# Performance work log

Measured on AMD Instinct MI355X. Metric: run time of the kernel, lower is better.

Reference implementation:

```python
import jax, jax.numpy as jnp
import numpy as np

N, E, FE, H, G, L, OUT = 50000, 300000, 64, 256, 256, 4, 128
BN_EPS = 1e-5


def setup_inputs() -> dict:
    key = jax.random.key(0)
    ks = jax.random.split(key, 12)
    s = 0.05
    return dict(
        x=jax.random.normal(ks[0], (N, H), jnp.float32),
        edge_index=jax.random.randint(ks[1], (2, E), 0, N, dtype=jnp.int64),
        edge_attr=jax.random.normal(ks[2], (E, FE), jnp.float32),
        batch=jnp.sort(jax.random.randint(ks[3], (N,), 0, G, dtype=jnp.int64)),
        bond_W1=jax.random.normal(ks[4], (L, FE, H), jnp.float32) * s,
        bond_b1=jnp.zeros((L, H), jnp.float32),
        bond_W2=jax.random.normal(ks[5], (L, H, H), jnp.float32) * s,
        bond_b2=jnp.zeros((L, H), jnp.float32),
        mlp_W1=jax.random.normal(ks[6], (L, H, H), jnp.float32) * s,
        mlp_b1=jnp.zeros((L, H), jnp.float32),
        mlp_W2=jax.random.normal(ks[7], (L, H, H), jnp.float32) * s,
        mlp_b2=jnp.zeros((L, H), jnp.float32),
        eps=jnp.zeros((L,), jnp.float32),
        bn_gamma=jnp.ones((L, H), jnp.float32),
        bn_beta=jnp.zeros((L, H), jnp.float32),
        fc1_W=jax.random.normal(ks[8], (L * H, H), jnp.float32) * s,
        fc1_b=jnp.zeros((H,), jnp.float32),
        fc4_W=jax.random.normal(ks[9], (H, OUT), jnp.float32) * s,
        fc4_b=jnp.zeros((OUT,), jnp.float32),
    )


def reference(x, edge_index, edge_attr, batch,
              bond_W1, bond_b1, bond_W2, bond_b2,
              mlp_W1, mlp_b1, mlp_W2, mlp_b2,
              eps, bn_gamma, bn_beta,
              fc1_W, fc1_b, fc4_W, fc4_b):
    src, dst = edge_index[0], edge_index[1]  # x_j gathered from src, scatter-add to dst
    x_lst = []
    for l in range(L):
        # bond encoder: Linear -> ReLU -> Linear on edge features [E, FE] -> [E, H]
        e = jax.nn.relu(edge_attr @ bond_W1[l] + bond_b1[l]) @ bond_W2[l] + bond_b2[l]
        # message = relu(x_j + e), aggregate = scatter-add over destination nodes
        msg = jax.nn.relu(x[src] + e)  # [E, H]
        aggr = jax.ops.segment_sum(msg, dst, num_segments=N)  # [N, H]
        h = (1.0 + eps[l]) * x + aggr
        h = jax.nn.relu(h @ mlp_W1[l] + mlp_b1[l]) @ mlp_W2[l] + mlp_b2[l]
        h = jax.nn.relu(h)
        # BatchNorm over the node dimension (training-style batch statistics)
        mu = jnp.mean(h, axis=0)
        var = jnp.var(h, axis=0)
        x = (h - mu) * jax.lax.rsqrt(var + BN_EPS) * bn_gamma[l] + bn_beta[l]
        x_lst.append(x)
    xc = jnp.concatenate(x_lst, axis=-1)  # [N, L*H]
    # global mean pool over graphs
    sums = jax.ops.segment_sum(xc, batch, num_segments=G)  # [G, L*H]
    cnts = jax.ops.segment_sum(jnp.ones((N,), xc.dtype), batch, num_segments=G)
    pooled = sums / jnp.maximum(cnts, 1.0)[:, None]
    h = jax.nn.relu(pooled @ fc1_W + fc1_b)
    # dropout p=0.5 in eval mode -> identity
    return h @ fc4_W + fc4_b  # [G, OUT]
```

## Files before the change

### kernel.cpp

```cpp
#include <hip/hip_runtime.h>

#define NN 50000
#define NE 300000
#define FEA 64
#define HD 256
#define NG 256
#define NL 4
#define OD 128
#define SCB ((NN + 255) / 256)

typedef unsigned short u16;
typedef unsigned int u32;
typedef __attribute__((ext_vector_type(8))) short short8;
typedef __attribute__((ext_vector_type(4))) float f32x4;

__device__ __forceinline__ u16 f2h(float f) {
    union { _Float16 h; u16 u; } v; v.h = (_Float16)f; return v.u;
}
__device__ __forceinline__ float h2f(u16 u) {
    union { u16 u; _Float16 h; } v; v.u = u; return (float)v.h;
}

__global__ __launch_bounds__(256, 2) void edge_k(
    const u16* __restrict__ eattrS, const u16* __restrict__ W1t,
    const float* __restrict__ bb1, const u16* __restrict__ W2t,
    const float* __restrict__ bb2,
    const int* __restrict__ srcI, const int* __restrict__ dstI,
    const u16* __restrict__ xh, float* __restrict__ aggr)
{
    __shared__ __align__(16) u16 bufW[256 * 64];
    __shared__ __align__(16) u16 bufT[64 * 256];
    __shared__ int dstL[64];
    const int tid = threadIdx.x;
    const int lane = tid & 63;
    const int w = tid >> 6;
    const int q = lane >> 4, c15 = lane & 15;
    const int e0 = blockIdx.x * 64;

#pragma unroll
    for (int it = 0; it < 2; ++it) {
        const int i = it * 256 + tid;
        const int m = i >> 3, kb = i & 7;
        int row = e0 + m; if (row > NE - 1) row = NE - 1;
        *(short8*)&bufT[m * 64 + ((kb ^ (m & 7)) * 8)] =
            *(const short8*)(eattrS + (size_t)row * FEA + kb * 8);
    }
#pragma unroll
    for (int it = 0; it < 8; ++it) {
        const int i = it * 256 + tid;
        const int n = i >> 3, kb = i & 7;
        *(short8*)&bufW[n * 64 + ((kb ^ (n & 7)) * 8)] =
            *(const short8*)(W1t + (size_t)n * FEA + kb * 8);
    }
    if (tid < 64) {
        int er = e0 + tid;
        dstL[tid] = (er < NE) ? dstI[er] : -1;
    }
    __syncthreads();

    f32x4 acc1[4][4];
#pragma unroll
    for (int i = 0; i < 4; ++i)
#pragma unroll
        for (int j = 0; j < 4; ++j) acc1[i][j] = (f32x4)0.0f;
#pragma unroll
    for (int s = 0; s < 2; ++s) {
        short8 af[4], bf[4];
#pragma unroll
        for (int t = 0; t < 4; ++t) {
            const int kga = s * 4 + q;
            const int mm = t * 16 + c15;
            af[t] = *(const short8*)&bufT[mm * 64 + ((kga ^ (mm & 7)) * 8)];
            const int nn = w * 64 + t * 16 + c15;
            bf[t] = *(const short8*)&bufW[nn * 64 + ((kga ^ (nn & 7)) * 8)];
        }
#pragma unroll
        for (int tm = 0; tm < 4; ++tm)
#pragma unroll
            for (int tn = 0; tn < 4; ++tn)
                acc1[tm][tn] = __builtin_amdgcn_mfma_f32_16x16x32_f16(
                    af[tm], bf[tn], acc1[tm][tn], 0, 0, 0);
    }
    __syncthreads();

    {
        float b1f[4];
#pragma unroll
        for (int tn = 0; tn < 4; ++tn)
            b1f[tn] = bb1[w * 64 + tn * 16 + c15];
#pragma unroll
        for (int tm = 0; tm < 4; ++tm)
#pragma unroll
            for (int tn = 0; tn < 4; ++tn) {
                const int col = w * 64 + tn * 16 + c15;
                const int kb = col >> 3;
#pragma unroll
                for (int r = 0; r < 4; ++r) {
                    const int row = tm * 16 + q * 4 + r;
                    float v = acc1[tm][tn][r] + b1f[tn];
                    v = v > 0.0f ? v : 0.0f;
                    bufT[row * 256 + ((kb ^ (row & 7)) * 8) + (col & 7)] = f2h(v);
                }
            }
    }

    f32x4 acc2[4][4];
#pragma unroll
    for (int i = 0; i < 4; ++i)
#pragma unroll
        for (int j = 0; j < 4; ++j) acc2[i][j] = (f32x4)0.0f;
    for (int k0 = 0; k0 < 256; k0 += 64) {
#pragma unroll
        for (int it = 0; it < 8; ++it) {
            const int i = it * 256 + tid;
            const int n = i >> 3, kbl = i & 7;
            *(short8*)&bufW[n * 64 + ((kbl ^ (n & 7)) * 8)] =
                *(const short8*)(W2t + (size_t)n * HD + k0 + kbl * 8);
        }
        __syncthreads();
#pragma unroll
        for (int s = 0; s < 2; ++s) {
            short8 af[4], bf[4];
#pragma unroll
            for (int t = 0; t < 4; ++t) {
                const int mm = t * 16 + c15;
                const int kbg = (k0 >> 3) + s * 4 + q;
                af[t] = *(const short8*)&bufT[mm * 256 + ((kbg ^ (mm & 7)) * 8)];
                const int nn = w * 64 + t * 16 + c15;
                const int kga = s * 4 + q;
                bf[t] = *(const short8*)&bufW[nn * 64 + ((kga ^ (nn & 7)) * 8)];
            }
#pragma unroll
            for (int tm = 0; tm < 4; ++tm)
#pragma unroll
                for (int tn = 0; tn < 4; ++tn)
                    acc2[tm][tn] = __builtin_amdgcn_mfma_f32_16x16x32_f16(
                        af[tm], bf[tn], acc2[tm][tn], 0, 0, 0);
        }
        __syncthreads();
    }

#pragma unroll
    for (int it = 0; it < 8; ++it) {
        const int idx = it * 256 + tid;
        const int row = idx >> 5;
        const int ch = idx & 31;
        int er = e0 + row; if (er > NE - 1) er = NE - 1;
        const int sn = srcI[er];
        *(short8*)&bufW[row * 256 + ch * 8] =
            *(const short8*)(xh + (size_t)sn * HD + ch * 8);
    }
    __syncthreads();

    {
        float b2f[4];
#pragma unroll
        for (int tn = 0; tn < 4; ++tn)
            b2f[tn] = bb2[w * 64 + tn * 16 + c15];
#pragma unroll
        for (int tm = 0; tm < 4; ++tm)
#pragma unroll
            for (int r = 0; r < 4; ++r) {
                const int row = tm * 16 + q * 4 + r;
                if (e0 + row < NE) {
#pragma unroll
                    for (int tn = 0; tn < 4; ++tn) {
                        const int col = w * 64 + tn * 16 + c15;
                        float v = acc2[tm][tn][r] + b2f[tn]
                                + h2f(bufW[row * 256 + col]);
                        v = v > 0.0f ? v : 0.0f;
                        bufT[row * 256 + col] = f2h(v);
                    }
                }
            }
    }
    __syncthreads();

    {
        const int hiR = (NE - e0 < 64) ? (NE - e0) : 64;
        float s = 0.0f;
        int cur = dstL[0];
        for (int rI = 0; rI < hiR; ++rI) {
            const int d = dstL[rI];
            if (d != cur) {
                if (s != 0.0f) unsafeAtomicAdd(&aggr[(size_t)cur * HD + tid], s);
                cur = d; s = 0.0f;
            }
            s += h2f(bufT[rI * 256 + tid]);
        }
        if (cur >= 0 && s != 0.0f)
            unsafeAtomicAdd(&aggr[(size_t)cur * HD + tid], s);
    }
}

__global__ __launch_bounds__(256, 2) void node_k(
    const u16* __restrict__ xh, const float* __restrict__ aggr,
    const float* __restrict__ epsv, int l,
    const u16* __restrict__ M1t, const float* __restrict__ mb1,
    const u16* __restrict__ M2t, const float* __restrict__ mb2,
    u16* __restrict__ hb, float* __restrict__ bns, float* __restrict__ bnq)
{
    __shared__ __align__(16) u16 bufW[256 * 64];
    __shared__ __align__(16) u16 bufT[64 * 256];
    const int tid = threadIdx.x;
    const int lane = tid & 63;
    const int w = tid >> 6;
    const int q = lane >> 4, c15 = lane & 15;
    const int n0b = blockIdx.x * 64;
    const float e1 = 1.0f + epsv[l];

#pragma unroll
    for (int it = 0; it < 8; ++it) {
        const int i = it * 256 + tid;
        const int m = i >> 5, kb = i & 31;
        int row = n0b + m; if (row > NN - 1) row = NN - 1;
        const size_t base = (size_t)row * HD + kb * 8;
        short8 xv = *(const short8*)(xh + base);
        float4 a0 = *(const float4*)(aggr + base);
        float4 a1 = *(const float4*)(aggr + base + 4);
        u16 o[8];
        o[0] = f2h(e1 * h2f((u16)xv[0]) + a0.x);
        o[1] = f2h(e1 * h2f((u16)xv[1]) + a0.y);
        o[2] = f2h(e1 * h2f((u16)xv[2]) + a0.z);
        o[3] = f2h(e1 * h2f((u16)xv[3]) + a0.w);
        o[4] = f2h(e1 * h2f((u16)xv[4]) + a1.x);
        o[5] = f2h(e1 * h2f((u16)xv[5]) + a1.y);
        o[6] = f2h(e1 * h2f((u16)xv[6]) + a1.z);
        o[7] = f2h(e1 * h2f((u16)xv[7]) + a1.w);
        *(short8*)&bufT[m * 256 + ((kb ^ (m & 7)) * 8)] = *(short8*)o;
    }

    f32x4 acc1[4][4];
#pragma unroll
    for (int i = 0; i < 4; ++i)
#pragma unroll
        for (int j = 0; j < 4; ++j) acc1[i][j] = (f32x4)0.0f;
    for (int k0 = 0; k0 < 256; k0 += 64) {
#pragma unroll
        for (int it = 0; it < 8; ++it) {
            const int i = it * 256 + tid;
            const int n = i >> 3, kbl = i & 7;
            *(short8*)&bufW[n * 64 + ((kbl ^ (n & 7)) * 8)] =
                *(const short8*)(M1t + (size_t)n * HD + k0 + kbl * 8);
        }
        __syncthreads();
#pragma unroll
        for (int s = 0; s < 2; ++s) {
            short8 af[4], bf[4];
#pragma unroll
            for (int t = 0; t < 4; ++t) {
                const int mm = t * 16 + c15;
                const int kbg = (k0 >> 3) + s * 4 + q;
                af[t] = *(const short8*)&bufT[mm * 256 + ((kbg ^ (mm & 7)) * 8)];
                const int nn = w * 64 + t * 16 + c15;
                const int kga = s * 4 + q;
                bf[t] = *(const short8*)&bufW[nn * 64 + ((kga ^ (nn & 7)) * 8)];
            }
#pragma unroll
            for (int tm = 0; tm < 4; ++tm)
#pragma unroll
                for (int tn = 0; tn < 4; ++tn)
                    acc1[tm][tn] = __builtin_amdgcn_mfma_f32_16x16x32_f16(
                        af[tm], bf[tn], acc1[tm][tn], 0, 0, 0);
        }
        __syncthreads();
    }

    {
        float b1f[4];
#pragma unroll
        for (int tn = 0; tn < 4; ++tn)
            b1f[tn] = mb1[w * 64 + tn * 16 + c15];
#pragma unroll
        for (int tm = 0; tm < 4; ++tm)
#pragma unroll
            for (int tn = 0; tn < 4; ++tn) {
                const int col = w * 64 + tn * 16 + c15;
                const int kb = col >> 3;
#pragma unroll
                for (int r = 0; r < 4; ++r) {
                    const int row = tm * 16 + q * 4 + r;
                    float v = acc1[tm][tn][r] + b1f[tn];
                    v = v > 0.0f ? v : 0.0f;
                    bufT[row * 256 + ((kb ^ (row & 7)) * 8) + (col & 7)] = f2h(v);
                }
            }
    }

    f32x4 acc2[4][4];
#pragma unroll
    for (int i = 0; i < 4; ++i)
#pragma unroll
        for (int j = 0; j < 4; ++j) acc2[i][j] = (f32x4)0.0f;
    for (int k0 = 0; k0 < 256; k0 += 64) {
#pragma unroll
        for (int it = 0; it < 8; ++it) {
            const int i = it * 256 + tid;
            const int n = i >> 3, kbl = i & 7;
            *(short8*)&bufW[n * 64 + ((kbl ^ (n & 7)) * 8)] =
                *(const short8*)(M2t + (size_t)n * HD + k0 + kbl * 8);
        }
        __syncthreads();
#pragma unroll
        for (int s = 0; s < 2; ++s) {
            short8 af[4], bf[4];
#pragma unroll
            for (int t = 0; t < 4; ++t) {
                const int mm = t * 16 + c15;
                const int kbg = (k0 >> 3) + s * 4 + q;
                af[t] = *(const short8*)&bufT[mm * 256 + ((kbg ^ (mm & 7)) * 8)];
                const int nn = w * 64 + t * 16 + c15;
                const int kga = s * 4 + q;
                bf[t] = *(const short8*)&bufW[nn * 64 + ((kga ^ (nn & 7)) * 8)];
            }
#pragma unroll
            for (int tm = 0; tm < 4; ++tm)
#pragma unroll
                for (int tn = 0; tn < 4; ++tn)
                    acc2[tm][tn] = __builtin_amdgcn_mfma_f32_16x16x32_f16(
                        af[tm], bf[tn], acc2[tm][tn], 0, 0, 0);
        }
        __syncthreads();
    }

    float b2f[4];
#pragma unroll
    for (int tn = 0; tn < 4; ++tn)
        b2f[tn] = mb2[w * 64 + tn * 16 + c15];
    float ps[4] = {0, 0, 0, 0}, pq[4] = {0, 0, 0, 0};
#pragma unroll
    for (int tm = 0; tm < 4; ++tm) {
#pragma unroll
        for (int r = 0; r < 4; ++r) {
            const int grow = n0b + tm * 16 + q * 4 + r;
            if (grow < NN) {
#pragma unroll
                for (int tn = 0; tn < 4; ++tn) {
                    const int col = w * 64 + tn * 16 + c15;
                    float v = acc2[tm][tn][r] + b2f[tn];
                    v = v > 0.0f ? v : 0.0f;
                    hb[(size_t)grow * HD + col] = f2h(v);
                    ps[tn] += v; pq[tn] += v * v;
                }
            }
        }
    }
#pragma unroll
    for (int tn = 0; tn < 4; ++tn) {
        float s = ps[tn], sq = pq[tn];
        s += __shfl_down(s, 32, 64);  sq += __shfl_down(sq, 32, 64);
        s += __shfl_down(s, 16, 64);  sq += __shfl_down(sq, 16, 64);
        if (q == 0) {
            const int col = w * 64 + tn * 16 + c15;
            unsafeAtomicAdd(&bns[col], s);
            unsafeAtomicAdd(&bnq[col], sq);
        }
    }
}


__global__ void transpose_k(const float* __restrict__ in, u16* __restrict__ oh,
                            int Kw, int Nw) {
    int i = blockIdx.x * blockDim.x + threadIdx.x;
    int tot = NL * Kw * Nw;
    if (i < tot) {
        int l = i / (Kw * Nw), rem = i % (Kw * Nw);
        int k = rem / Nw, n = rem % Nw;
        oh[(size_t)l * Kw * Nw + (size_t)n * Kw + k] = f2h(in[i]);
    }
}

__global__ void cvt_k(const float* __restrict__ in, u16* __restrict__ outh, int tot) {
    int i = blockIdx.x * blockDim.x + threadIdx.x;
    if (i < tot) outh[i] = f2h(in[i]);
}

__global__ void egather_k(const float* __restrict__ eattr, const int* __restrict__ perm,
                          u16* __restrict__ eattrS) {
    int i = blockIdx.x * blockDim.x + threadIdx.x;
    if (i < NE * FEA) {
        int row = i >> 6, k = i & 63;
        eattrS[i] = f2h(eattr[(size_t)perm[row] * FEA + k]);
    }
}

__global__ void zero_layer_k(float* __restrict__ aggr, float* __restrict__ bns,
                             float* __restrict__ bnq) {
    int i = blockIdx.x * blockDim.x + threadIdx.x;
    if (i < NN * HD) aggr[i] = 0.0f;
    if (i < HD) { bns[i] = 0.0f; bnq[i] = 0.0f; }
}

__global__ void bnfin_k(const float* __restrict__ bns, const float* __restrict__ bnq,
                        const float* __restrict__ gamma, const float* __restrict__ beta,
                        int l, float* __restrict__ ab) {
    int c = threadIdx.x;
    float mu = bns[c] * (1.0f / (float)NN);
    float var = bnq[c] * (1.0f / (float)NN) - mu * mu;
    if (var < 0.0f) var = 0.0f;
    float a = gamma[l * HD + c] * rsqrtf(var + 1e-5f);
    float b = beta[l * HD + c] - mu * a;
    ab[c] = a; ab[HD + c] = b;
}

__global__ void bnapply_k(const u16* __restrict__ hb, const float* __restrict__ ab,
                          u16* __restrict__ xh) {
    int i = blockIdx.x * blockDim.x + threadIdx.x;
    if (i < NN * HD) {
        int c = i & (HD - 1);
        xh[i] = f2h(ab[c] * h2f(hb[i]) + ab[HD + c]);
    }
}


__global__ void zeroi_k(int* __restrict__ a, int n) {
    int i = blockIdx.x * blockDim.x + threadIdx.x;
    if (i < n) a[i] = 0;
}

__global__ void hist_k(const int* __restrict__ dst, int* __restrict__ hist) {
    int e = blockIdx.x * blockDim.x + threadIdx.x;
    if (e < NE) atomicAdd(&hist[dst[e]], 1);
}

__global__ void sumblk_k(const int* __restrict__ hist, int* __restrict__ psum) {
    __shared__ int red[256];
    int b = blockIdx.x, t = threadIdx.x, i = b * 256 + t;
    red[t] = (i < NN) ? hist[i] : 0;
    __syncthreads();
    for (int o = 128; o > 0; o >>= 1) {
        if (t < o) red[t] += red[t + o];
        __syncthreads();
    }
    if (t == 0) psum[b] = red[0];
}

__global__ void scanblk_k(int* __restrict__ psum) {
    __shared__ int sc[256];
    int t = threadIdx.x;
    int v = (t < SCB) ? psum[t] : 0;
    sc[t] = v; __syncthreads();
    for (int o = 1; o < 256; o <<= 1) {
        int x = (t >= o) ? sc[t - o] : 0;
        __syncthreads(); sc[t] += x; __syncthreads();
    }
    if (t < SCB) psum[t] = sc[t] - v;
}

__global__ void scanfin_k(const int* __restrict__ hist, const int* __restrict__ psum,
                          int* __restrict__ rowptr) {
    __shared__ int sc[256];
    int b = blockIdx.x, t = threadIdx.x, i = b * 256 + t;
    int v = (i < NN) ? hist[i] : 0;
    sc[t] = v; __syncthreads();
    for (int o = 1; o < 256; o <<= 1) {
        int x = (t >= o) ? sc[t - o] : 0;
        __syncthreads(); sc[t] += x; __syncthreads();
    }
    if (i < NN) rowptr[i] = psum[b] + sc[t] - v;
    if (i == NN - 1) rowptr[NN] = psum[b] + sc[t];
}

__global__ void copyi_k(const int* __restrict__ src, int* __restrict__ dst, int n) {
    int i = blockIdx.x * blockDim.x + threadIdx.x;
    if (i < n) dst[i] = src[i];
}

__global__ void scatter_k(const int* __restrict__ dst, int* __restrict__ next,
                          int* __restrict__ perm) {
    int e = blockIdx.x * blockDim.x + threadIdx.x;
    if (e < NE) {
        int p = atomicAdd(&next[dst[e]], 1);
        perm[p] = e;
    }
}

__global__ void permsd_k(const int* __restrict__ eidx, const int* __restrict__ perm,
                         int* __restrict__ srcS, int* __restrict__ dstS) {
    int i = blockIdx.x * blockDim.x + threadIdx.x;
    if (i < NE) {
        int e = perm[i];
        srcS[i] = eidx[e];
        dstS[i] = eidx[NE + e];
    }
}


__global__ void zcnt_k(int* __restrict__ cnts) {
    if (threadIdx.x < NG) cnts[threadIdx.x] = 0;
}

__global__ void count_k(const int* __restrict__ batch, int* __restrict__ cnts) {
    int i = blockIdx.x * blockDim.x + threadIdx.x;
    if (i < NN) atomicAdd(&cnts[batch[i]], 1);
}

__global__ void offs_k(const int* __restrict__ cnts, int* __restrict__ offs) {
    if (threadIdx.x == 0) {
        int a = 0;
        for (int g = 0; g < NG; ++g) { offs[g] = a; a += cnts[g]; }
        offs[NG] = a;
    }
}

__global__ void pool_layer_k(const u16* __restrict__ xh, const int* __restrict__ offs,
                             float* __restrict__ pooled, int l) {
    int g = blockIdx.x, t = threadIdx.x;
    int lo = offs[g], hi = offs[g + 1];
    float s = 0.0f;
    for (int n = lo; n < hi; ++n) s += h2f(xh[(size_t)n * HD + t]);
    int c = hi - lo; if (c < 1) c = 1;
    pooled[(size_t)g * (NL * HD) + l * HD + t] = s / (float)c;
}

__global__ void fc_k(const float* __restrict__ pooled,
                     const float* __restrict__ W1, const float* __restrict__ b1,
                     const float* __restrict__ W4, const float* __restrict__ b4,
                     float* __restrict__ out) {
    __shared__ float pl[NL * HD];
    __shared__ float hm[HD];
    int g = blockIdx.x, t = threadIdx.x;
#pragma unroll
    for (int j = 0; j < 4; ++j) pl[t + j * 256] = pooled[(size_t)g * 1024 + t + j * 256];
    __syncthreads();
    float a = b1[t];
    for (int k = 0; k < 1024; ++k) a += pl[k] * W1[k * 256 + t];
    hm[t] = a > 0.0f ? a : 0.0f;
    __syncthreads();
    if (t < OD) {
        float o = b4[t];
        for (int k = 0; k < 256; ++k) o += hm[k] * W4[k * OD + t];
        out[g * OD + t] = o;
    }
}


extern "C" void kernel_launch(void* const* d_in, const int* in_sizes, int n_in,
                              void* d_out, int out_size, void* d_ws, size_t ws_size,
                              hipStream_t stream) {
    const float* x_in  = (const float*)d_in[0];
    const int*   eidx  = (const int*)d_in[1];
    const float* eattr = (const float*)d_in[2];
    const int*   batch = (const int*)d_in[3];
    const float* bW1   = (const float*)d_in[4];
    const float* bb1   = (const float*)d_in[5];
    const float* bW2   = (const float*)d_in[6];
    const float* bb2   = (const float*)d_in[7];
    const float* mW1   = (const float*)d_in[8];
    const float* mb1   = (const float*)d_in[9];
    const float* mW2   = (const float*)d_in[10];
    const float* mb2   = (const float*)d_in[11];
    const float* epsv  = (const float*)d_in[12];
    const float* gamma = (const float*)d_in[13];
    const float* beta  = (const float*)d_in[14];
    const float* fc1W  = (const float*)d_in[15];
    const float* fc1b  = (const float*)d_in[16];
    const float* fc4W  = (const float*)d_in[17];
    const float* fc4b  = (const float*)d_in[18];
    float* out = (float*)d_out;
    (void)in_sizes; (void)n_in; (void)out_size; (void)ws_size;

    size_t off = 0;
    auto alloc = [&](size_t bytes) -> char* {
        char* r = (char*)d_ws + off;
        off = (off + bytes + 255) & ~(size_t)255;
        return r;
    };
    u16*   xh   = (u16*)alloc((size_t)NN * HD * 2);
    float* aggr = (float*)alloc((size_t)NN * HD * 4);
    u16*   hb   = (u16*)alloc((size_t)NN * HD * 2);
    u16*   eattrS = (u16*)alloc((size_t)NE * FEA * 2);
    u16*   W1t  = (u16*)alloc((size_t)NL * FEA * HD * 2);
    u16*   W2t  = (u16*)alloc((size_t)NL * HD * HD * 2);
    u16*   M1t  = (u16*)alloc((size_t)NL * HD * HD * 2);
    u16*   M2t  = (u16*)alloc((size_t)NL * HD * HD * 2);
    float* bns  = (float*)alloc(HD * 4);
    float* bnq  = (float*)alloc(HD * 4);
    float* ab   = (float*)alloc(2 * HD * 4);
    int*   cnts = (int*)alloc(NG * 4);
    int*   offs = (int*)alloc((NG + 1) * 4);
    float* pooled = (float*)alloc((size_t)NG * NL * HD * 4);
    int*   hist  = (int*)alloc((size_t)NN * 4);
    int*   psum  = (int*)alloc((size_t)SCB * 4);
    int*   rowptr = (int*)alloc((size_t)(NN + 1) * 4);
    int*   perm  = (int*)alloc((size_t)NE * 4);
    int*   srcS  = (int*)alloc((size_t)NE * 4);
    int*   dstS  = (int*)alloc((size_t)NE * 4);

    const int NEL = NN * HD;
    const int EB = (NEL + 255) / 256;
    const int NEB = (NE + 255) / 256;

    transpose_k<<<(NL * FEA * HD + 255) / 256, 256, 0, stream>>>(bW1, W1t, FEA, HD);
    transpose_k<<<(NL * HD * HD + 255) / 256, 256, 0, stream>>>(bW2, W2t, HD, HD);
    transpose_k<<<(NL * HD * HD + 255) / 256, 256, 0, stream>>>(mW1, M1t, HD, HD);
    transpose_k<<<(NL * HD * HD + 255) / 256, 256, 0, stream>>>(mW2, M2t, HD, HD);

    cvt_k<<<EB, 256, 0, stream>>>(x_in, xh, NEL);

    zeroi_k<<<(NN + 255) / 256, 256, 0, stream>>>(hist, NN);
    hist_k<<<NEB, 256, 0, stream>>>(eidx + NE, hist);
    sumblk_k<<<SCB, 256, 0, stream>>>(hist, psum);
    scanblk_k<<<1, 256, 0, stream>>>(psum);
    scanfin_k<<<SCB, 256, 0, stream>>>(hist, psum, rowptr);
    copyi_k<<<(NN + 255) / 256, 256, 0, stream>>>(rowptr, hist, NN);
    scatter_k<<<NEB, 256, 0, stream>>>(eidx + NE, hist, perm);
    permsd_k<<<NEB, 256, 0, stream>>>(eidx, perm, srcS, dstS);
    egather_k<<<(NE * FEA + 255) / 256, 256, 0, stream>>>(eattr, perm, eattrS);

    zcnt_k<<<1, 256, 0, stream>>>(cnts);
    count_k<<<(NN + 255) / 256, 256, 0, stream>>>(batch, cnts);
    offs_k<<<1, 64, 0, stream>>>(cnts, offs);

    const int EGB = (NE + 63) / 64;
    const int NGB = (NN + 63) / 64;

    for (int l = 0; l < NL; ++l) {
        zero_layer_k<<<EB, 256, 0, stream>>>(aggr, bns, bnq);
        edge_k<<<EGB, 256, 0, stream>>>(
            eattrS, W1t + (size_t)l * FEA * HD, bb1 + l * HD,
            W2t + (size_t)l * HD * HD, bb2 + l * HD,
            srcS, dstS, xh, aggr);
        node_k<<<NGB, 256, 0, stream>>>(
            xh, aggr, epsv, l,
            M1t + (size_t)l * HD * HD, mb1 + l * HD,
            M2t + (size_t)l * HD * HD, mb2 + l * HD,
            hb, bns, bnq);
        bnfin_k<<<1, HD, 0, stream>>>(bns, bnq, gamma, beta, l, ab);
        bnapply_k<<<EB, 256, 0, stream>>>(hb, ab, xh);
        pool_layer_k<<<NG, HD, 0, stream>>>(xh, offs, pooled, l);
    }
    fc_k<<<NG, 256, 0, stream>>>(pooled, fc1W, fc1b, fc4W, fc4b, out);
}
```

Measured before the change: 1.557 ms.

## Double-buffer weight staging via direct global-to-LDS loads and fuse pooling into BN apply

The edge and node GEMM kernels now stage weight tiles with global_load_lds straight into LDS, using 32-wide K chunks that are double-buffered so the next chunk loads while MFMAs run on the current one. The x[src] gather is overlapped with the last K chunk, and s_setprio is raised around the MFMA bursts. Separately, mean pooling is folded into the BN-apply kernel through per-graph atomics, with division by the count deferred to fc_k, which removes pool_layer_k and offs_k. The cost is more barriers, float atomic-order nondeterminism in pooling, and per-row batch lookups in bnapply.

```diff
diff --git a/kernel.cpp b/kernel.cpp
--- a/kernel.cpp
+++ b/kernel.cpp
@@ -19,6 +19,12 @@
 }
 __device__ __forceinline__ float h2f(u16 u) {
     union { u16 u; _Float16 h; } v; v.u = u; return (float)v.h;
+}
+
+typedef const __attribute__((address_space(1))) unsigned int gas_u32;
+typedef __attribute__((address_space(3))) unsigned int las_u32;
+__device__ __forceinline__ void gld16(const void* g, void* l) {
+    __builtin_amdgcn_global_load_lds((gas_u32*)g, (las_u32*)l, 16, 0, 0);
 }
 
 __global__ __launch_bounds__(256, 2) void edge_k(
@@ -31,30 +37,34 @@
     __shared__ __align__(16) u16 bufW[256 * 64];
     __shared__ __align__(16) u16 bufT[64 * 256];
     __shared__ int dstL[64];
+    __shared__ int srcL[64];
     const int tid = threadIdx.x;
     const int lane = tid & 63;
     const int w = tid >> 6;
     const int q = lane >> 4, c15 = lane & 15;
     const int e0 = blockIdx.x * 64;
-
+    const int wb = tid & ~63;
+
+    if (tid < 64) {
+        int er = e0 + tid;
+        int erc = er < NE ? er : NE - 1;
+        dstL[tid] = (er < NE) ? dstI[erc] : -1;
+        srcL[tid] = srcI[erc];
+    }
 #pragma unroll
     for (int it = 0; it < 2; ++it) {
         const int i = it * 256 + tid;
         const int m = i >> 3, kb = i & 7;
         int row = e0 + m; if (row > NE - 1) row = NE - 1;
-        *(short8*)&bufT[m * 64 + ((kb ^ (m & 7)) * 8)] =
-            *(const short8*)(eattrS + (size_t)row * FEA + kb * 8);
+        gld16(eattrS + (size_t)row * FEA + ((kb ^ (m & 7)) * 8),
+              &bufT[(it * 256 + wb) * 8]);
     }
 #pragma unroll
     for (int it = 0; it < 8; ++it) {
         const int i = it * 256 + tid;
         const int n = i >> 3, kb = i & 7;
-        *(short8*)&bufW[n * 64 + ((kb ^ (n & 7)) * 8)] =
-            *(const short8*)(W1t + (size_t)n * FEA + kb * 8);
-    }
-    if (tid < 64) {
-        int er = e0 + tid;
-        dstL[tid] = (er < NE) ? dstI[er] : -1;
+        gld16(W1t + (size_t)n * FEA + ((kb ^ (n & 7)) * 8),
+              &bufW[(it * 256 + wb) * 8]);
     }
     __syncthreads();
 
@@ -74,14 +84,29 @@
             const int nn = w * 64 + t * 16 + c15;
             bf[t] = *(const short8*)&bufW[nn * 64 + ((kga ^ (nn & 7)) * 8)];
         }
+        __builtin_amdgcn_s_setprio(1);
 #pragma unroll
         for (int tm = 0; tm < 4; ++tm)
 #pragma unroll
             for (int tn = 0; tn < 4; ++tn)
                 acc1[tm][tn] = __builtin_amdgcn_mfma_f32_16x16x32_f16(
                     af[tm], bf[tn], acc1[tm][tn], 0, 0, 0);
-    }
-    __syncthreads();
+        __builtin_amdgcn_s_setprio(0);
+    }
+    __syncthreads();
+
+    auto stageW2 = [&](int cc) {
+        const int k0c = cc * 32;
+        const int hB = (cc & 1) * 1024;
+#pragma unroll
+        for (int it = 0; it < 4; ++it) {
+            const int i = it * 256 + tid;
+            const int n = i >> 2, j = i & 3;
+            gld16(W2t + (size_t)n * HD + k0c + ((j ^ ((n >> 1) & 3)) * 8),
+                  &bufW[(hB + it * 256 + wb) * 8]);
+        }
+    };
+    stageW2(0);
 
     {
         float b1f[4];
@@ -103,77 +128,76 @@
                 }
             }
     }
+    __syncthreads();
 
     f32x4 acc2[4][4];
 #pragma unroll
     for (int i = 0; i < 4; ++i)
 #pragma unroll
         for (int j = 0; j < 4; ++j) acc2[i][j] = (f32x4)0.0f;
-    for (int k0 = 0; k0 < 256; k0 += 64) {
-#pragma unroll
-        for (int it = 0; it < 8; ++it) {
-            const int i = it * 256 + tid;
-            const int n = i >> 3, kbl = i & 7;
-            *(short8*)&bufW[n * 64 + ((kbl ^ (n & 7)) * 8)] =
-                *(const short8*)(W2t + (size_t)n * HD + k0 + kbl * 8);
-        }
+#pragma unroll
+    for (int c = 0; c < 8; ++c) {
+        if (c < 7) {
+            stageW2(c + 1);
+        } else {
+#pragma unroll
+            for (int it = 0; it < 4; ++it) {
+                const int i = it * 256 + tid;
+                const int row = i >> 5, ch = i & 31;
+                gld16(xh + (size_t)srcL[row] * HD + ch * 8,
+                      &bufW[(it * 256 + wb) * 8]);
+            }
+        }
+        short8 af[4], bf[4];
+        const u16* hp = &bufW[(c & 1) * 8192];
+#pragma unroll
+        for (int t = 0; t < 4; ++t) {
+            const int mm = t * 16 + c15;
+            const int kbg = c * 4 + q;
+            af[t] = *(const short8*)&bufT[mm * 256 + ((kbg ^ (mm & 7)) * 8)];
+            const int nn = w * 64 + t * 16 + c15;
+            bf[t] = *(const short8*)&hp[nn * 32 + ((q ^ ((nn >> 1) & 3)) * 8)];
+        }
+        __builtin_amdgcn_s_setprio(1);
+#pragma unroll
+        for (int tm = 0; tm < 4; ++tm)
+#pragma unroll
+            for (int tn = 0; tn < 4; ++tn)
+                acc2[tm][tn] = __builtin_amdgcn_mfma_f32_16x16x32_f16(
+                    af[tm], bf[tn], acc2[tm][tn], 0, 0, 0);
+        __builtin_amdgcn_s_setprio(0);
         __syncthreads();
-#pragma unroll
-        for (int s = 0; s < 2; ++s) {
-            short8 af[4], bf[4];
-#pragma unroll
-            for (int t = 0; t < 4; ++t) {
-                const int mm = t * 16 + c15;
-                const int kbg = (k0 >> 3) + s * 4 + q;
-                af[t] = *(const short8*)&bufT[mm * 256 + ((kbg ^ (mm & 7)) * 8)];
-                const int nn = w * 64 + t * 16 + c15;
-                const int kga = s * 4 + q;
-                bf[t] = *(const short8*)&bufW[nn * 64 + ((kga ^ (nn & 7)) * 8)];
-            }
-#pragma unroll
-            for (int tm = 0; tm < 4; ++tm)
-#pragma unroll
-                for (int tn = 0; tn < 4; ++tn)
-                    acc2[tm][tn] = __builtin_amdgcn_mfma_f32_16x16x32_f16(
-                        af[tm], bf[tn], acc2[tm][tn], 0, 0, 0);
-        }
-        __syncthreads();
-    }
-
-#pragma unroll
-    for (int it = 0; it < 8; ++it) {
-        const int idx = it * 256 + tid;
-        const int row = idx >> 5;
-        const int ch = idx & 31;
-        int er = e0 + row; if (er > NE - 1) er = NE - 1;
-        const int sn = srcI[er];
-        *(short8*)&bufW[row * 256 + ch * 8] =
-            *(const short8*)(xh + (size_t)sn * HD + ch * 8);
-    }
-    __syncthreads();
-
-    {
-        float b2f[4];
-#pragma unroll
-        for (int tn = 0; tn < 4; ++tn)
-            b2f[tn] = bb2[w * 64 + tn * 16 + c15];
-#pragma unroll
-        for (int tm = 0; tm < 4; ++tm)
-#pragma unroll
-            for (int r = 0; r < 4; ++r) {
-                const int row = tm * 16 + q * 4 + r;
-                if (e0 + row < NE) {
-#pragma unroll
-                    for (int tn = 0; tn < 4; ++tn) {
-                        const int col = w * 64 + tn * 16 + c15;
-                        float v = acc2[tm][tn][r] + b2f[tn]
-                                + h2f(bufW[row * 256 + col]);
-                        v = v > 0.0f ? v : 0.0f;
-                        bufT[row * 256 + col] = f2h(v);
-                    }
+    }
+
+#pragma unroll
+    for (int it = 0; it < 4; ++it) {
+        const int i = 1024 + it * 256 + tid;
+        const int row = i >> 5, ch = i & 31;
+        gld16(xh + (size_t)srcL[row] * HD + ch * 8,
+              &bufW[(1024 + it * 256 + wb) * 8]);
+    }
+    float b2f[4];
+#pragma unroll
+    for (int tn = 0; tn < 4; ++tn)
+        b2f[tn] = bb2[w * 64 + tn * 16 + c15];
+    __syncthreads();
+
+#pragma unroll
+    for (int tm = 0; tm < 4; ++tm)
+#pragma unroll
+        for (int r = 0; r < 4; ++r) {
+            const int row = tm * 16 + q * 4 + r;
+            if (e0 + row < NE) {
+#pragma unroll
+                for (int tn = 0; tn < 4; ++tn) {
+                    const int col = w * 64 + tn * 16 + c15;
+                    float v = acc2[tm][tn][r] + b2f[tn]
+                            + h2f(bufW[row * 256 + col]);
+                    v = v > 0.0f ? v : 0.0f;
+                    bufT[row * 256 + col] = f2h(v);
                 }
             }
-    }
+        }
     __syncthreads();
 
     {
@@ -208,6 +232,20 @@
     const int q = lane >> 4, c15 = lane & 15;
     const int n0b = blockIdx.x * 64;
     const float e1 = 1.0f + epsv[l];
+    const int wb = tid & ~63;
+
+    auto stageM = [&](const u16* Mt, int cc) {
+        const int k0c = cc * 32;
+        const int hB = (cc & 1) * 1024;
+#pragma unroll
+        for (int it = 0; it < 4; ++it) {
+            const int i = it * 256 + tid;
+            const int n = i >> 2, j = i & 3;
+            gld16(Mt + (size_t)n * HD + k0c + ((j ^ ((n >> 1) & 3)) * 8),
+                  &bufW[(hB + it * 256 + wb) * 8]);
+        }
+    };
+    stageM(M1t, 0);
 
 #pragma unroll
     for (int it = 0; it < 8; ++it) {
@@ -229,40 +267,35 @@
         o[7] = f2h(e1 * h2f((u16)xv[7]) + a1.w);
         *(short8*)&bufT[m * 256 + ((kb ^ (m & 7)) * 8)] = *(short8*)o;
     }
+    __syncthreads();
 
     f32x4 acc1[4][4];
 #pragma unroll
     for (int i = 0; i < 4; ++i)
 #pragma unroll
         for (int j = 0; j < 4; ++j) acc1[i][j] = (f32x4)0.0f;
-    for (int k0 = 0; k0 < 256; k0 += 64) {
-#pragma unroll
-        for (int it = 0; it < 8; ++it) {
-            const int i = it * 256 + tid;
-            const int n = i >> 3, kbl = i & 7;
-            *(short8*)&bufW[n * 64 + ((kbl ^ (n & 7)) * 8)] =
-                *(const short8*)(M1t + (size_t)n * HD + k0 + kbl * 8);
-        }
-        __syncthreads();
-#pragma unroll
-        for (int s = 0; s < 2; ++s) {
-            short8 af[4], bf[4];
-#pragma unroll
-            for (int t = 0; t < 4; ++t) {
-                const int mm = t * 16 + c15;
-                const int kbg = (k0 >> 3) + s * 4 + q;
-                af[t] = *(const short8*)&bufT[mm * 256 + ((kbg ^ (mm & 7)) * 8)];
-                const int nn = w * 64 + t * 16 + c15;
-                const int kga = s * 4 + q;
-                bf[t] = *(const short8*)&bufW[nn * 64 + ((kga ^ (nn & 7)) * 8)];
-            }
-#pragma unroll
-            for (int tm = 0; tm < 4; ++tm)
-#pragma unroll
-                for (int tn = 0; tn < 4; ++tn)
-                    acc1[tm][tn] = __builtin_amdgcn_mfma_f32_16x16x32_f16(
-                        af[tm], bf[tn], acc1[tm][tn], 0, 0, 0);
-        }
+#pragma unroll
+    for (int c = 0; c < 8; ++c) {
+        if (c < 7) stageM(M1t, c + 1);
+        else       stageM(M2t, 0);
+        short8 af[4], bf[4];
+        const u16* hp = &bufW[(c & 1) * 8192];
+#pragma unroll
+        for (int t = 0; t < 4; ++t) {
+            const int mm = t * 16 + c15;
+            const int kbg = c * 4 + q;
+            af[t] = *(const short8*)&bufT[mm * 256 + ((kbg ^ (mm & 7)) * 8)];
+            const int nn = w * 64 + t * 16 + c15;
+            bf[t] = *(const short8*)&hp[nn * 32 + ((q ^ ((nn >> 1) & 3)) * 8)];
+        }
+        __builtin_amdgcn_s_setprio(1);
+#pragma unroll
+        for (int tm = 0; tm < 4; ++tm)
+#pragma unroll
+            for (int tn = 0; tn < 4; ++tn)
+                acc1[tm][tn] = __builtin_amdgcn_mfma_f32_16x16x32_f16(
+                    af[tm], bf[tn], acc1[tm][tn], 0, 0, 0);
+        __builtin_amdgcn_s_setprio(0);
         __syncthreads();
     }
 
@@ -286,40 +319,34 @@
                 }
             }
     }
+    __syncthreads();
 
     f32x4 acc2[4][4];
 #pragma unroll
     for (int i = 0; i < 4; ++i)
 #pragma unroll
         for (int j = 0; j < 4; ++j) acc2[i][j] = (f32x4)0.0f;
-    for (int k0 = 0; k0 < 256; k0 += 64) {
-#pragma unroll
-        for (int it = 0; it < 8; ++it) {
-            const int i = it * 256 + tid;
-            const int n = i >> 3, kbl = i & 7;
-            *(short8*)&bufW[n * 64 + ((kbl ^ (n & 7)) * 8)] =
-                *(const short8*)(M2t + (size_t)n * HD + k0 + kbl * 8);
-        }
-        __syncthreads();
-#pragma unroll
-        for (int s = 0; s < 2; ++s) {
-            short8 af[4], bf[4];
-#pragma unroll
-            for (int t = 0; t < 4; ++t) {
-                const int mm = t * 16 + c15;
-                const int kbg = (k0 >> 3) + s * 4 + q;
-                af[t] = *(const short8*)&bufT[mm * 256 + ((kbg ^ (mm & 7)) * 8)];
-                const int nn = w * 64 + t * 16 + c15;
-                const int kga = s * 4 + q;
-                bf[t] = *(const short8*)&bufW[nn * 64 + ((kga ^ (nn & 7)) * 8)];
-            }
-#pragma unroll
-            for (int tm = 0; tm < 4; ++tm)
-#pragma unroll
-                for (int tn = 0; tn < 4; ++tn)
-                    acc2[tm][tn] = __builtin_amdgcn_mfma_f32_16x16x32_f16(
-                        af[tm], bf[tn], acc2[tm][tn], 0, 0, 0);
-        }
+#pragma unroll
+    for (int c = 0; c < 8; ++c) {
+        if (c < 7) stageM(M2t, c + 1);
+        short8 af[4], bf[4];
+        const u16* hp = &bufW[(c & 1) * 8192];
+#pragma unroll
+        for (int t = 0; t < 4; ++t) {
+            const int mm = t * 16 + c15;
+            const int kbg = c * 4 + q;
+            af[t] = *(const short8*)&bufT[mm * 256 + ((kbg ^ (mm & 7)) * 8)];
+            const int nn = w * 64 + t * 16 + c15;
+            bf[t] = *(const short8*)&hp[nn * 32 + ((q ^ ((nn >> 1) & 3)) * 8)];
+        }
+        __builtin_amdgcn_s_setprio(1);
+#pragma unroll
+        for (int tm = 0; tm < 4; ++tm)
+#pragma unroll
+            for (int tn = 0; tn < 4; ++tn)
+                acc2[tm][tn] = __builtin_amdgcn_mfma_f32_16x16x32_f16(
+                    af[tm], bf[tn], acc2[tm][tn], 0, 0, 0);
+        __builtin_amdgcn_s_setprio(0);
         __syncthreads();
     }
 
@@ -389,6 +416,11 @@
     int i = blockIdx.x * blockDim.x + threadIdx.x;
     if (i < NN * HD) aggr[i] = 0.0f;
     if (i < HD) { bns[i] = 0.0f; bnq[i] = 0.0f; }
+}
+
+__global__ void zerof_k(float* __restrict__ p, int n) {
+    int i = blockIdx.x * blockDim.x + threadIdx.x;
+    if (i < n) p[i] = 0.0f;
 }
 
 __global__ void bnfin_k(const float* __restrict__ bns, const float* __restrict__ bnq,
@@ -404,12 +436,26 @@
 }
 
 __global__ void bnapply_k(const u16* __restrict__ hb, const float* __restrict__ ab,
-                          u16* __restrict__ xh) {
-    int i = blockIdx.x * blockDim.x + threadIdx.x;
-    if (i < NN * HD) {
-        int c = i & (HD - 1);
-        xh[i] = f2h(ab[c] * h2f(hb[i]) + ab[HD + c]);
-    }
+                          const int* __restrict__ batch, u16* __restrict__ xh,
+                          float* __restrict__ pooled, int l) {
+    const int t = threadIdx.x;
+    const int n0 = blockIdx.x * 64;
+    const float a = ab[t], b = ab[HD + t];
+    const int hi = (NN - n0 < 64) ? (NN - n0) : 64;
+    float s = 0.0f;
+    int cur = batch[n0];
+    for (int r = 0; r < hi; ++r) {
+        const size_t idx = (size_t)(n0 + r) * HD + t;
+        float v = a * h2f(hb[idx]) + b;
+        xh[idx] = f2h(v);
+        const int g = batch[n0 + r];
+        if (g != cur) {
+            unsafeAtomicAdd(&pooled[(size_t)cur * (NL * HD) + l * HD + t], s);
+            s = 0.0f; cur = g;
+        }
+        s += v;
+    }
+    unsafeAtomicAdd(&pooled[(size_t)cur * (NL * HD) + l * HD + t], s);
 }
 
 
@@ -495,33 +541,17 @@
     if (i < NN) atomicAdd(&cnts[batch[i]], 1);
 }
 
-__global__ void offs_k(const int* __restrict__ cnts, int* __restrict__ offs) {
-    if (threadIdx.x == 0) {
-        int a = 0;
-        for (int g = 0; g < NG; ++g) { offs[g] = a; a += cnts[g]; }
-        offs[NG] = a;
-    }
-}
-
-__global__ void pool_layer_k(const u16* __restrict__ xh, const int* __restrict__ offs,
-                             float* __restrict__ pooled, int l) {
-    int g = blockIdx.x, t = threadIdx.x;
-    int lo = offs[g], hi = offs[g + 1];
-    float s = 0.0f;
-    for (int n = lo; n < hi; ++n) s += h2f(xh[(size_t)n * HD + t]);
-    int c = hi - lo; if (c < 1) c = 1;
-    pooled[(size_t)g * (NL * HD) + l * HD + t] = s / (float)c;
-}
-
-__global__ void fc_k(const float* __restrict__ pooled,
+__global__ void fc_k(const float* __restrict__ pooled, const int* __restrict__ cnts,
                      const float* __restrict__ W1, const float* __restrict__ b1,
                      const float* __restrict__ W4, const float* __restrict__ b4,
                      float* __restrict__ out) {
     __shared__ float pl[NL * HD];
     __shared__ float hm[HD];
     int g = blockIdx.x, t = threadIdx.x;
-#pragma unroll
-    for (int j = 0; j < 4; ++j) pl[t + j * 256] = pooled[(size_t)g * 1024 + t + j * 256];
+    const float inv = 1.0f / fmaxf((float)cnts[g], 1.0f);
+#pragma unroll
+    for (int j = 0; j < 4; ++j)
+        pl[t + j * 256] = pooled[(size_t)g * 1024 + t + j * 256] * inv;
     __syncthreads();
     float a = b1[t];
     for (int k = 0; k < 1024; ++k) a += pl[k] * W1[k * 256 + t];
@@ -578,7 +608,6 @@
     float* bnq  = (float*)alloc(HD * 4);
     float* ab   = (float*)alloc(2 * HD * 4);
     int*   cnts = (int*)alloc(NG * 4);
-    int*   offs = (int*)alloc((NG + 1) * 4);
     float* pooled = (float*)alloc((size_t)NG * NL * HD * 4);
     int*   hist  = (int*)alloc((size_t)NN * 4);
     int*   psum  = (int*)alloc((size_t)SCB * 4);
@@ -610,7 +639,7 @@
 
     zcnt_k<<<1, 256, 0, stream>>>(cnts);
     count_k<<<(NN + 255) / 256, 256, 0, stream>>>(batch, cnts);
-    offs_k<<<1, 64, 0, stream>>>(cnts, offs);
+    zerof_k<<<(NG * NL * HD + 255) / 256, 256, 0, stream>>>(pooled, NG * NL * HD);
 
     const int EGB = (NE + 63) / 64;
     const int NGB = (NN + 63) / 64;
@@ -627,8 +656,7 @@
             M2t + (size_t)l * HD * HD, mb2 + l * HD,
             hb, bns, bnq);
         bnfin_k<<<1, HD, 0, stream>>>(bns, bnq, gamma, beta, l, ab);
-        bnapply_k<<<EB, 256, 0, stream>>>(hb, ab, xh);
-        pool_layer_k<<<NG, HD, 0, stream>>>(xh, offs, pooled, l);
-    }
-    fc_k<<<NG, 256, 0, stream>>>(pooled, fc1W, fc1b, fc4W, fc4b, out);
-}
+        bnapply_k<<<NGB, 256, 0, stream>>>(hb, ab, batch, xh, pooled, l);
+    }
+    fc_k<<<NG, 256, 0, stream>>>(pooled, cnts, fc1W, fc1b, fc4W, fc4b, out);
+}
```

New measurement: 1.342 ms. 1.16x faster.
